# Kernel tuning notes

Measured on AMD Instinct MI355X. Metric: run time of the kernel, lower is better.

Reference implementation:

```python
import jax, jax.numpy as jnp
import numpy as np

B, N, T, L, H = 8, 128, 256, 32, 128


def setup_inputs() -> dict:
    key = jax.random.key(0)
    k0, k1, k2, k3, k4, k5 = jax.random.split(key, 6)
    x = jax.random.uniform(k0, (B, N, T), dtype=jnp.float32)
    s = 1.0 / np.sqrt(H)  # pytorch LSTM/Linear default init scale
    W_ih = jax.random.uniform(k1, (N, 4 * H, L), minval=-s, maxval=s, dtype=jnp.float32)
    b_ih = jax.random.uniform(k2, (N, 4 * H), minval=-s, maxval=s, dtype=jnp.float32)
    b_hh = jax.random.uniform(k3, (N, 4 * H), minval=-s, maxval=s, dtype=jnp.float32)
    W_fc = jax.random.uniform(k4, (N, N, H), minval=-s, maxval=s, dtype=jnp.float32)  # [node_i, out_j, H]
    b_fc = jax.random.uniform(k5, (N, N), minval=-s, maxval=s, dtype=jnp.float32)  # [node_i, out_j]
    return {"x": x, "W_ih": W_ih, "b_ih": b_ih, "b_hh": b_hh, "W_fc": W_fc, "b_fc": b_fc}


def reference(x, W_ih, b_ih, b_hh, W_fc, b_fc):
    # x: [B, N, T]
    Bn, Nn, Tn = x.shape
    Ln = W_ih.shape[-1]
    Hh = W_fc.shape[-1]
    Ttau = Tn - Ln  # number of prediction steps (t = L .. T-1)

    # Sliding windows x[:, i, tau:tau+L] for tau = 0..Ttau-1  -> [B, N, Ttau, L]
    idx = jnp.arange(Ttau)[:, None] + jnp.arange(Ln)[None, :]  # [Ttau, L]
    xw = x[:, :, idx]

    # Single-step LSTM with zero initial state: W_hh term vanishes.
    gates = jnp.einsum('bntl,ngl->bntg', xw, W_ih) + (b_ih + b_hh)[None, :, None, :]
    gi, gf, gg, go = jnp.split(gates, 4, axis=-1)  # pytorch order: i, f, g, o
    c = jax.nn.sigmoid(gi) * jnp.tanh(gg)          # f*c0 = 0
    h = jax.nn.sigmoid(go) * jnp.tanh(c)           # [B, N, Ttau, H]

    # Per-node fc (grouped GEMM): contributions[b, tau, j, i]
    contrib = jnp.einsum('bnth,njh->btjn', h, W_fc) + b_fc.T[None, None, :, :]

    # G[b, j, i] = mean_tau contrib[b, tau, j, i] / x[b, i, L + tau]
    denom = jnp.transpose(x[:, :, Ln:], (0, 2, 1))[:, :, None, :]  # [B, Ttau, 1, N_i]
    G = jnp.mean(contrib / denom, axis=1)                          # [B, N, N]

    X_hat = jnp.sum(contrib, axis=2) + 1e-6  # [B, Ttau, N]
    return G, X_hat
```

## Files before the change

### kernel.cpp

```cpp
#include <hip/hip_runtime.h>
#include <math.h>

#define B_  8
#define N_  128
#define T_  256
#define L_  32
#define H_  128
#define TT_ 224

typedef float f2    __attribute__((ext_vector_type(2)));
typedef float f4    __attribute__((ext_vector_type(4)));
typedef float f32x4 __attribute__((ext_vector_type(4)));
typedef short bf16x8 __attribute__((ext_vector_type(8)));

#define L2E_  1.4426950408889634f
#define L2E2_ 2.8853900817779268f

__device__ __forceinline__ unsigned pk2bf(float a, float b) {
    unsigned ua = __float_as_uint(a), ub = __float_as_uint(b);
    ua = (ua + 0x7FFFu + ((ua >> 16) & 1u)) >> 16;
    ub = (ub + 0x7FFFu + ((ub >> 16) & 1u)) >> 16;
    return ua | (ub << 16);
}
__device__ __forceinline__ float aexp2(float x) {
    float r; asm("v_exp_f32 %0, %1" : "=v"(r) : "v"(x)); return r;
}
__device__ __forceinline__ float aexp2n(float x) {
    float r; asm("v_exp_f32 %0, -%1" : "=v"(r) : "v"(x)); return r;
}
__device__ __forceinline__ float arcp(float x) {
    return __builtin_amdgcn_rcpf(x);
}

__global__ __launch_bounds__(256)
__attribute__((amdgpu_waves_per_eu(4, 4)))
void k_main(const float* __restrict__ x,
            const float* __restrict__ W_ih,
            const float* __restrict__ b_ih, const float* __restrict__ b_hh,
            const float* __restrict__ W_fc, const float* __restrict__ b_fc,
            float* __restrict__ G, float* __restrict__ xhat) {
    const int n   = blockIdx.x;
    const int b   = blockIdx.y;
    const int tid = threadIdx.x;
    const int w    = tid >> 6;
    const int lane = tid & 63;
    const int col  = lane & 15;
    const int quad = lane >> 4;

    __shared__ __attribute__((aligned(16))) float xs[260];
    __shared__ __attribute__((aligned(16))) unsigned xeo[2][128];
    __shared__ __attribute__((aligned(16))) float xr[TT_];
    __shared__ uint4 xA[14 * 64];
    __shared__ __attribute__((aligned(16))) float xh_part[4][TT_];
    __shared__ __attribute__((aligned(16))) float hd_loc[H_];
    __shared__ float red[4];
    __shared__ f4 wpart[8][32];
    __shared__ f4 ws4[32];
    __shared__ float bp[2];
    __shared__ float bs_s;

    union { uint4 u; bf16x8 v; } bfr[2][3];
    f32x4 biaR[2][3];
    #pragma unroll
    for (int ht2 = 0; ht2 < 2; ++ht2) {
        const int ht = 2 * w + ht2;
        const int hb = ht * 16 + quad * 4;
        #pragma unroll
        for (int g = 0; g < 3; ++g) {
            const int r  = g * 128 + ht * 16 + col;
            const int sr = r + (r >= 128 ? 128 : 0);
            const float sc = (g == 1) ? L2E2_ : L2E_;
            const f4* src = (const f4*)(W_ih + (size_t)n * 512 * L_ +
                                        (size_t)sr * L_ + quad * 8);
            f4 v0 = src[0] * sc, v1 = src[1] * sc;
            bfr[ht2][g].u.x = pk2bf(v0.x, v0.y);
            bfr[ht2][g].u.y = pk2bf(v0.z, v0.w);
            bfr[ht2][g].u.z = pk2bf(v1.x, v1.y);
            bfr[ht2][g].u.w = pk2bf(v1.z, v1.w);
            const int sg = (g == 0) ? 0 : (g == 1 ? 256 : 384);
            const f4 bi = *(const f4*)&b_ih[(size_t)n * 512 + sg + hb];
            const f4 bh = *(const f4*)&b_hh[(size_t)n * 512 + sg + hb];
            const f4 bs = (bi + bh) * sc;
            biaR[ht2][g][0] = bs.x; biaR[ht2][g][1] = bs.y;
            biaR[ht2][g][2] = bs.z; biaR[ht2][g][3] = bs.w;
        }
    }
    {
        const int h4 = tid & 31, jg = tid >> 5;
        const f4* Wf = (const f4*)(W_fc + (size_t)n * N_ * H_) +
                       (size_t)jg * 16 * 32 + h4;
        f4 s = {0.f, 0.f, 0.f, 0.f};
        #pragma unroll
        for (int j = 0; j < 16; ++j) s += Wf[j * 32];
        wpart[jg][h4] = s;
    }
    if (tid < 128) {
        float bv = b_fc[n * N_ + tid];
        #pragma unroll
        for (int off = 32; off > 0; off >>= 1) bv += __shfl_down(bv, off, 64);
        if ((tid & 63) == 0) bp[tid >> 6] = bv;
    }
    xs[tid] = x[((size_t)b * N_ + n) * T_ + tid];
    if (tid < 4) xs[256 + tid] = 0.f;
    __syncthreads();

    if (tid < TT_) xr[tid] = 1.0f / xs[L_ + tid];
    if (tid < 128) {
        xeo[0][tid] = pk2bf(xs[2 * tid],     xs[2 * tid + 1]);
        xeo[1][tid] = pk2bf(xs[2 * tid + 1], xs[2 * tid + 2]);
    }
    if (tid < 32) {
        f4 s = wpart[0][tid];
        #pragma unroll
        for (int jg = 1; jg < 8; ++jg) s += wpart[jg][tid];
        ws4[tid] = s;
    }
    if (tid == 0) bs_s = bp[0] + bp[1];
    __syncthreads();

    for (int e = tid; e < 14 * 64; e += 256) {
        const int tt = e >> 6, ln = e & 63;
        const int s  = tt * 16 + (ln & 15) + (ln >> 4) * 8;
        const int p  = s & 1, base = s >> 1;
        uint4 v;
        v.x = xeo[p][base + 0]; v.y = xeo[p][base + 1];
        v.z = xeo[p][base + 2]; v.w = xeo[p][base + 3];
        xA[e] = v;
    }
    __syncthreads();

    f4 wshF[2];
    #pragma unroll
    for (int ht2 = 0; ht2 < 2; ++ht2) {
        const int hb = (2 * w + ht2) * 16 + quad * 4;
        wshF[ht2] = ws4[hb >> 2];
    }
    const float bsum_n = bs_s;

    f32x4 hdacc[2] = {{0.f,0.f,0.f,0.f},{0.f,0.f,0.f,0.f}};
    const f32x4 zero4 = {0.f, 0.f, 0.f, 0.f};

    #pragma unroll 2
    for (int ttile = 0; ttile < 14; ++ttile) {
        union { uint4 u; bf16x8 v; } af;
        af.u = xA[ttile * 64 + lane];
        const float xrt = xr[ttile * 16 + col];

        float xsum = 0.f;
        #pragma unroll
        for (int ht2 = 0; ht2 < 2; ++ht2) {
            f32x4 gi = __builtin_amdgcn_mfma_f32_16x16x32_bf16(bfr[ht2][0].v, af.v, zero4, 0, 0, 0);
            f32x4 gg = __builtin_amdgcn_mfma_f32_16x16x32_bf16(bfr[ht2][1].v, af.v, zero4, 0, 0, 0);
            f32x4 go = __builtin_amdgcn_mfma_f32_16x16x32_bf16(bfr[ht2][2].v, af.v, zero4, 0, 0, 0);
            gi += biaR[ht2][0];
            gg += biaR[ht2][1];
            go += biaR[ht2][2];

            f32x4 e1, e2, e3;
            #pragma unroll
            for (int r = 0; r < 4; ++r) {
                e1[r] = aexp2n(gi[r]);
                e2[r] = aexp2(gg[r]);
                e3[r] = aexp2n(go[r]);
            }
            const f32x4 A  = (1.f + e1) * (e2 + 1.f);
            const f32x4 Bv = 1.f + e3;
            const f32x4 AB = A * Bv;
            f32x4 R;
            #pragma unroll
            for (int r = 0; r < 4; ++r) R[r] = arcp(AB[r]);
            const f32x4 em = e2 - 1.f;
            const f32x4 t  = em * R;
            const f32x4 c  = t * Bv;
            const f32x4 c2 = c * c;
            f32x4 Q = c2 * -0.027698f + 0.120833f;
            Q = c2 * Q - 0.331541f;
            Q = c2 * Q + 1.0f;
            const f32x4 hh = t * Q;

            hdacc[ht2] += hh * xrt;
            xsum = fmaf(hh[0], wshF[ht2][0],
                   fmaf(hh[1], wshF[ht2][1],
                   fmaf(hh[2], wshF[ht2][2],
                   fmaf(hh[3], wshF[ht2][3], xsum))));
        }
        xsum += __shfl_xor(xsum, 16, 64);
        xsum += __shfl_xor(xsum, 32, 64);
        if (lane < 16) xh_part[w][ttile * 16 + lane] = xsum;
    }

    #pragma unroll
    for (int ht2 = 0; ht2 < 2; ++ht2) {
        #pragma unroll
        for (int r = 0; r < 4; ++r) {
            float v = hdacc[ht2][r];
            v += __shfl_xor(v, 1, 64);
            v += __shfl_xor(v, 2, 64);
            v += __shfl_xor(v, 4, 64);
            v += __shfl_xor(v, 8, 64);
            if (col == 0) hd_loc[(2 * w + ht2) * 16 + quad * 4 + r] = v;
        }
    }
    {
        float dv = (tid < TT_) ? xr[tid] : 0.f;
        #pragma unroll
        for (int off = 32; off > 0; off >>= 1) dv += __shfl_down(dv, off, 64);
        if (lane == 0) red[w] = dv;
    }
    __syncthreads();

    if (tid < TT_) {
        const float v = xh_part[0][tid] + xh_part[1][tid] +
                        xh_part[2][tid] + xh_part[3][tid];
        xhat[((size_t)b * TT_ + tid) * N_ + n] = v + bsum_n + 1e-6f;
    }

    {
        const float dinv = red[0] + red[1] + red[2] + red[3];
        const int j    = tid >> 1;
        const int half = tid & 1;
        const f4* Wf = (const f4*)(W_fc + ((size_t)n * N_ + j) * H_ + half * 64);
        float s = 0.f;
        #pragma unroll
        for (int q = 0; q < 16; ++q) {
            const f4 wv = Wf[q];
            const int hb = half * 64 + q * 4;
            s = fmaf(wv.x, hd_loc[hb + 0],
                fmaf(wv.y, hd_loc[hb + 1],
                fmaf(wv.z, hd_loc[hb + 2],
                fmaf(wv.w, hd_loc[hb + 3], s))));
        }
        s += __shfl_xor(s, 1, 64);
        if (half == 0) {
            const float bj = b_fc[n * N_ + j];
            G[(size_t)b * N_ * N_ + (size_t)j * N_ + n] =
                (s + bj * dinv) * (1.0f / 224.0f);
        }
    }
}

extern "C" void kernel_launch(void* const* d_in, const int* in_sizes, int n_in,
                              void* d_out, int out_size, void* d_ws, size_t ws_size,
                              hipStream_t stream) {
    const float* x    = (const float*)d_in[0];
    const float* W_ih = (const float*)d_in[1];
    const float* b_ih = (const float*)d_in[2];
    const float* b_hh = (const float*)d_in[3];
    const float* W_fc = (const float*)d_in[4];
    const float* b_fc = (const float*)d_in[5];

    float* G    = (float*)d_out;
    float* xhat = (float*)d_out + (size_t)B_ * N_ * N_;

    (void)d_ws; (void)ws_size;

    k_main<<<dim3(N_, B_), dim3(256), 0, stream>>>(x, W_ih, b_ih, b_hh,
                                                   W_fc, b_fc, G, xhat);
}
```

Measured before the change: 109.3 us.

## Double block size to 512 threads with one hidden tile per wave

Each block now runs 8 waves instead of 4, and each wave handles a single 16-wide hidden tile instead of two. The W_fc partial sums, the xhat partial reductions and the G dot products are re-split across the larger thread count, and the wpart scratch now reuses the xA shared buffer. The aim is more latency hiding and parallelism per block across MFMA and transcendental work. The cost is duplicated per-wave setup and extra reduction work, plus different occupancy under launch_bounds(512,8).

```diff
diff --git a/kernel.cpp b/kernel.cpp
--- a/kernel.cpp
+++ b/kernel.cpp
@@ -32,8 +32,7 @@
     return __builtin_amdgcn_rcpf(x);
 }
 
-__global__ __launch_bounds__(256)
-__attribute__((amdgpu_waves_per_eu(4, 4)))
+__global__ __launch_bounds__(512, 8)
 void k_main(const float* __restrict__ x,
             const float* __restrict__ W_ih,
             const float* __restrict__ b_ih, const float* __restrict__ b_hh,
@@ -51,19 +50,19 @@
     __shared__ __attribute__((aligned(16))) unsigned xeo[2][128];
     __shared__ __attribute__((aligned(16))) float xr[TT_];
     __shared__ uint4 xA[14 * 64];
-    __shared__ __attribute__((aligned(16))) float xh_part[4][TT_];
+    __shared__ __attribute__((aligned(16))) float xh_part[8][TT_];
     __shared__ __attribute__((aligned(16))) float hd_loc[H_];
-    __shared__ float red[4];
-    __shared__ f4 wpart[8][32];
+    __shared__ float red[8];
     __shared__ f4 ws4[32];
     __shared__ float bp[2];
     __shared__ float bs_s;
 
-    union { uint4 u; bf16x8 v; } bfr[2][3];
-    f32x4 biaR[2][3];
-    #pragma unroll
-    for (int ht2 = 0; ht2 < 2; ++ht2) {
-        const int ht = 2 * w + ht2;
+    f4* wpart = (f4*)xA;
+
+    union { uint4 u; bf16x8 v; } bfr[3];
+    f32x4 biaR[3];
+    {
+        const int ht = w;
         const int hb = ht * 16 + quad * 4;
         #pragma unroll
         for (int g = 0; g < 3; ++g) {
@@ -73,26 +72,26 @@
             const f4* src = (const f4*)(W_ih + (size_t)n * 512 * L_ +
                                         (size_t)sr * L_ + quad * 8);
             f4 v0 = src[0] * sc, v1 = src[1] * sc;
-            bfr[ht2][g].u.x = pk2bf(v0.x, v0.y);
-            bfr[ht2][g].u.y = pk2bf(v0.z, v0.w);
-            bfr[ht2][g].u.z = pk2bf(v1.x, v1.y);
-            bfr[ht2][g].u.w = pk2bf(v1.z, v1.w);
+            bfr[g].u.x = pk2bf(v0.x, v0.y);
+            bfr[g].u.y = pk2bf(v0.z, v0.w);
+            bfr[g].u.z = pk2bf(v1.x, v1.y);
+            bfr[g].u.w = pk2bf(v1.z, v1.w);
             const int sg = (g == 0) ? 0 : (g == 1 ? 256 : 384);
             const f4 bi = *(const f4*)&b_ih[(size_t)n * 512 + sg + hb];
             const f4 bh = *(const f4*)&b_hh[(size_t)n * 512 + sg + hb];
             const f4 bs = (bi + bh) * sc;
-            biaR[ht2][g][0] = bs.x; biaR[ht2][g][1] = bs.y;
-            biaR[ht2][g][2] = bs.z; biaR[ht2][g][3] = bs.w;
+            biaR[g][0] = bs.x; biaR[g][1] = bs.y;
+            biaR[g][2] = bs.z; biaR[g][3] = bs.w;
         }
     }
     {
         const int h4 = tid & 31, jg = tid >> 5;
         const f4* Wf = (const f4*)(W_fc + (size_t)n * N_ * H_) +
-                       (size_t)jg * 16 * 32 + h4;
+                       (size_t)jg * 8 * 32 + h4;
         f4 s = {0.f, 0.f, 0.f, 0.f};
         #pragma unroll
-        for (int j = 0; j < 16; ++j) s += Wf[j * 32];
-        wpart[jg][h4] = s;
+        for (int j = 0; j < 8; ++j) s += Wf[j * 32];
+        wpart[jg * 32 + h4] = s;
     }
     if (tid < 128) {
         float bv = b_fc[n * N_ + tid];
@@ -100,8 +99,8 @@
         for (int off = 32; off > 0; off >>= 1) bv += __shfl_down(bv, off, 64);
         if ((tid & 63) == 0) bp[tid >> 6] = bv;
     }
-    xs[tid] = x[((size_t)b * N_ + n) * T_ + tid];
-    if (tid < 4) xs[256 + tid] = 0.f;
+    if (tid < 256) xs[tid] = x[((size_t)b * N_ + n) * T_ + tid];
+    if (tid < 4)   xs[256 + tid] = 0.f;
     __syncthreads();
 
     if (tid < TT_) xr[tid] = 1.0f / xs[L_ + tid];
@@ -110,15 +109,15 @@
         xeo[1][tid] = pk2bf(xs[2 * tid + 1], xs[2 * tid + 2]);
     }
     if (tid < 32) {
-        f4 s = wpart[0][tid];
-        #pragma unroll
-        for (int jg = 1; jg < 8; ++jg) s += wpart[jg][tid];
+        f4 s = wpart[tid];
+        #pragma unroll
+        for (int jg = 1; jg < 16; ++jg) s += wpart[jg * 32 + tid];
         ws4[tid] = s;
     }
     if (tid == 0) bs_s = bp[0] + bp[1];
     __syncthreads();
 
-    for (int e = tid; e < 14 * 64; e += 256) {
+    for (int e = tid; e < 14 * 64; e += 512) {
         const int tt = e >> 6, ln = e & 63;
         const int s  = tt * 16 + (ln & 15) + (ln >> 4) * 8;
         const int p  = s & 1, base = s >> 1;
@@ -129,77 +128,64 @@
     }
     __syncthreads();
 
-    f4 wshF[2];
-    #pragma unroll
-    for (int ht2 = 0; ht2 < 2; ++ht2) {
-        const int hb = (2 * w + ht2) * 16 + quad * 4;
-        wshF[ht2] = ws4[hb >> 2];
-    }
+    const f4 wshF = ws4[(w * 16 + quad * 4) >> 2];
     const float bsum_n = bs_s;
 
-    f32x4 hdacc[2] = {{0.f,0.f,0.f,0.f},{0.f,0.f,0.f,0.f}};
+    f32x4 hdacc = {0.f, 0.f, 0.f, 0.f};
     const f32x4 zero4 = {0.f, 0.f, 0.f, 0.f};
 
-    #pragma unroll 2
     for (int ttile = 0; ttile < 14; ++ttile) {
         union { uint4 u; bf16x8 v; } af;
         af.u = xA[ttile * 64 + lane];
         const float xrt = xr[ttile * 16 + col];
 
-        float xsum = 0.f;
-        #pragma unroll
-        for (int ht2 = 0; ht2 < 2; ++ht2) {
-            f32x4 gi = __builtin_amdgcn_mfma_f32_16x16x32_bf16(bfr[ht2][0].v, af.v, zero4, 0, 0, 0);
-            f32x4 gg = __builtin_amdgcn_mfma_f32_16x16x32_bf16(bfr[ht2][1].v, af.v, zero4, 0, 0, 0);
-            f32x4 go = __builtin_amdgcn_mfma_f32_16x16x32_bf16(bfr[ht2][2].v, af.v, zero4, 0, 0, 0);
-            gi += biaR[ht2][0];
-            gg += biaR[ht2][1];
-            go += biaR[ht2][2];
-
-            f32x4 e1, e2, e3;
-            #pragma unroll
-            for (int r = 0; r < 4; ++r) {
-                e1[r] = aexp2n(gi[r]);
-                e2[r] = aexp2(gg[r]);
-                e3[r] = aexp2n(go[r]);
-            }
-            const f32x4 A  = (1.f + e1) * (e2 + 1.f);
-            const f32x4 Bv = 1.f + e3;
-            const f32x4 AB = A * Bv;
-            f32x4 R;
-            #pragma unroll
-            for (int r = 0; r < 4; ++r) R[r] = arcp(AB[r]);
-            const f32x4 em = e2 - 1.f;
-            const f32x4 t  = em * R;
-            const f32x4 c  = t * Bv;
-            const f32x4 c2 = c * c;
-            f32x4 Q = c2 * -0.027698f + 0.120833f;
-            Q = c2 * Q - 0.331541f;
-            Q = c2 * Q + 1.0f;
-            const f32x4 hh = t * Q;
-
-            hdacc[ht2] += hh * xrt;
-            xsum = fmaf(hh[0], wshF[ht2][0],
-                   fmaf(hh[1], wshF[ht2][1],
-                   fmaf(hh[2], wshF[ht2][2],
-                   fmaf(hh[3], wshF[ht2][3], xsum))));
-        }
+        f32x4 gi = __builtin_amdgcn_mfma_f32_16x16x32_bf16(bfr[0].v, af.v, zero4, 0, 0, 0);
+        f32x4 gg = __builtin_amdgcn_mfma_f32_16x16x32_bf16(bfr[1].v, af.v, zero4, 0, 0, 0);
+        f32x4 go = __builtin_amdgcn_mfma_f32_16x16x32_bf16(bfr[2].v, af.v, zero4, 0, 0, 0);
+        gi += biaR[0];
+        gg += biaR[1];
+        go += biaR[2];
+
+        f32x4 e1, e2, e3;
+        #pragma unroll
+        for (int r = 0; r < 4; ++r) {
+            e1[r] = aexp2n(gi[r]);
+            e2[r] = aexp2(gg[r]);
+            e3[r] = aexp2n(go[r]);
+        }
+        const f32x4 A  = (1.f + e1) * (e2 + 1.f);
+        const f32x4 Bv = 1.f + e3;
+        const f32x4 AB = A * Bv;
+        f32x4 R;
+        #pragma unroll
+        for (int r = 0; r < 4; ++r) R[r] = arcp(AB[r]);
+        const f32x4 em = e2 - 1.f;
+        const f32x4 t  = em * R;
+        const f32x4 c  = t * Bv;
+        const f32x4 c2 = c * c;
+        f32x4 Q = c2 * -0.027698f + 0.120833f;
+        Q = c2 * Q - 0.331541f;
+        Q = c2 * Q + 1.0f;
+        const f32x4 hh = t * Q;
+
+        hdacc += hh * xrt;
+        float xsum = fmaf(hh[0], wshF.x,
+                     fmaf(hh[1], wshF.y,
+                     fmaf(hh[2], wshF.z,
+                     fmaf(hh[3], wshF.w, 0.f))));
         xsum += __shfl_xor(xsum, 16, 64);
         xsum += __shfl_xor(xsum, 32, 64);
         if (lane < 16) xh_part[w][ttile * 16 + lane] = xsum;
     }
 
     #pragma unroll
-    for (int ht2 = 0; ht2 < 2; ++ht2) {
-        #pragma unroll
-        for (int r = 0; r < 4; ++r) {
-            float v = hdacc[ht2][r];
-            v += __shfl_xor(v, 1, 64);
-            v += __shfl_xor(v, 2, 64);
-            v += __shfl_xor(v, 4, 64);
-            v += __shfl_xor(v, 8, 64);
-            if (col == 0) hd_loc[(2 * w + ht2) * 16 + quad * 4 + r] = v;
-        }
+    for (int r = 0; r < 4; ++r) {
+        float v = hdacc[r];
+        v += __shfl_xor(v, 1, 64);
+        v += __shfl_xor(v, 2, 64);
+        v += __shfl_xor(v, 4, 64);
+        v += __shfl_xor(v, 8, 64);
+        if (col == 0) hd_loc[w * 16 + quad * 4 + r] = v;
     }
     {
         float dv = (tid < TT_) ? xr[tid] : 0.f;
@@ -210,28 +196,32 @@
     __syncthreads();
 
     if (tid < TT_) {
-        const float v = xh_part[0][tid] + xh_part[1][tid] +
-                        xh_part[2][tid] + xh_part[3][tid];
+        const float v = (xh_part[0][tid] + xh_part[1][tid]) +
+                        (xh_part[2][tid] + xh_part[3][tid]) +
+                        (xh_part[4][tid] + xh_part[5][tid]) +
+                        (xh_part[6][tid] + xh_part[7][tid]);
         xhat[((size_t)b * TT_ + tid) * N_ + n] = v + bsum_n + 1e-6f;
     }
 
     {
-        const float dinv = red[0] + red[1] + red[2] + red[3];
-        const int j    = tid >> 1;
-        const int half = tid & 1;
-        const f4* Wf = (const f4*)(W_fc + ((size_t)n * N_ + j) * H_ + half * 64);
+        const float dinv = (red[0] + red[1]) + (red[2] + red[3]) +
+                           (red[4] + red[5]) + (red[6] + red[7]);
+        const int j   = tid >> 2;
+        const int qtr = tid & 3;
+        const f4* Wf = (const f4*)(W_fc + ((size_t)n * N_ + j) * H_ + qtr * 32);
         float s = 0.f;
         #pragma unroll
-        for (int q = 0; q < 16; ++q) {
+        for (int q = 0; q < 8; ++q) {
             const f4 wv = Wf[q];
-            const int hb = half * 64 + q * 4;
+            const int hb = qtr * 32 + q * 4;
             s = fmaf(wv.x, hd_loc[hb + 0],
                 fmaf(wv.y, hd_loc[hb + 1],
                 fmaf(wv.z, hd_loc[hb + 2],
                 fmaf(wv.w, hd_loc[hb + 3], s))));
         }
         s += __shfl_xor(s, 1, 64);
-        if (half == 0) {
+        s += __shfl_xor(s, 2, 64);
+        if (qtr == 0) {
             const float bj = b_fc[n * N_ + j];
             G[(size_t)b * N_ * N_ + (size_t)j * N_ + n] =
                 (s + bj * dinv) * (1.0f / 224.0f);
@@ -254,6 +244,6 @@
 
     (void)d_ws; (void)ws_size;
 
-    k_main<<<dim3(N_, B_), dim3(256), 0, stream>>>(x, W_ih, b_ih, b_hh,
+    k_main<<<dim3(N_, B_), dim3(512), 0, stream>>>(x, W_ih, b_ih, b_hh,
                                                    W_fc, b_fc, G, xhat);
 }
```

Result: no change. 109.8 us (+0.5%).
